# Kernel tuning notes

Measured on AMD Instinct MI355X. Metric: run time of the kernel, lower is better.

## Reference

```python
import jax, jax.numpy as jnp
import numpy as np

B, H, W, C = 8, 64, 64, 256
C8 = C // 8  # query/key channels


def setup_inputs() -> dict:
    key = jax.random.key(0)
    ks = jax.random.split(key, 8)
    s = 0.02  # init scale for weights
    return {
        "x": jax.random.normal(ks[0], (B, H, W, C), dtype=jnp.float32),
        "Wq": jax.random.normal(ks[1], (C, C8), dtype=jnp.float32) * s,
        "bq": jnp.zeros((C8,), dtype=jnp.float32),
        "Wk": jax.random.normal(ks[2], (C, C8), dtype=jnp.float32) * s,
        "bk": jnp.zeros((C8,), dtype=jnp.float32),
        "Wv": jax.random.normal(ks[3], (C, C), dtype=jnp.float32) * s,
        "bv": jnp.zeros((C,), dtype=jnp.float32),
        "gamma": jnp.full((1,), 0.5, dtype=jnp.float32),
    }


def reference(x, Wq, bq, Wk, bk, Wv, bv, gamma):
    Bn, Hn, Wn, Cn = x.shape
    N = Hn * Wn
    xf = x.reshape(Bn, N, Cn)            # flatten spatial dims: [B, N, C]
    # 1x1 convs == per-pixel dense projections over channels
    q = xf @ Wq + bq                     # [B, N, C//8]
    k = xf @ Wk + bk                     # [B, N, C//8]
    v = xf @ Wv + bv                     # [B, N, C]
    # energy[b,i,j] = k_i . q_j  (matches tf.matmul(key, query, transpose_b=True))
    energy = jnp.einsum('bic,bjc->bij', k, q)   # [B, N, N]
    attn = jax.nn.softmax(energy, axis=-1)      # softmax over last axis
    # out_i = sum_j attn[i,j] * v_j  (intended SAGAN aggregation in NHWC layout)
    out = jnp.einsum('bij,bjc->bic', attn, v)   # [B, N, C]
    out = out.reshape(Bn, Hn, Wn, Cn)
    return gamma * out + x
```

## Files before the change

kernel.cpp:

```cpp
#include <hip/hip_runtime.h>

typedef __attribute__((ext_vector_type(8))) short short8;
typedef __attribute__((ext_vector_type(4))) float f32x4;
typedef __attribute__((ext_vector_type(16))) float f32x16;
typedef __attribute__((ext_vector_type(2))) unsigned int u32x2;
typedef __attribute__((ext_vector_type(4))) unsigned int u32x4;
typedef unsigned short u16;
typedef unsigned int u32;

#define MFMA16(a, b, c) __builtin_amdgcn_mfma_f32_16x16x32_bf16((a), (b), (c), 0, 0, 0)
#define MFMA32(a, b, c) __builtin_amdgcn_mfma_f32_32x32x16_bf16((a), (b), (c), 0, 0, 0)

#define BAR_VMEM() asm volatile("s_waitcnt vmcnt(0) lgkmcnt(0)\ns_barrier" ::: "memory")
#define BAR_LDS()  asm volatile("s_waitcnt lgkmcnt(0)\ns_barrier" ::: "memory")

#define BATCH 8
#define NTOK 4096
#define CDIM 256
#define CQK 32
#define LOG2E 1.4426950408889634f

__device__ __forceinline__ u16 f2bf(float f) {
  u32 u = __float_as_uint(f);
  return (u16)((u + 0x7FFFu + ((u >> 16) & 1u)) >> 16);
}
__device__ __forceinline__ u32 pack2(float a, float b) {
  const u32 ua = __float_as_uint(a) + 0x8000u;
  const u32 ub = __float_as_uint(b) + 0x8000u;
#if __has_builtin(__builtin_amdgcn_perm)
  return __builtin_amdgcn_perm(ub, ua, 0x07060302u);
#else
  return (ua >> 16) | (ub & 0xFFFF0000u);
#endif
}
__device__ __forceinline__ float fexp2(float x) {
#if __has_builtin(__builtin_amdgcn_exp2f)
  return __builtin_amdgcn_exp2f(x);
#else
  return exp2f(x);
#endif
}
__device__ __forceinline__ void gl_lds16(const u16* g, u16* l) {
  __builtin_amdgcn_global_load_lds(
      (const __attribute__((address_space(1))) unsigned int*)(g),
      (__attribute__((address_space(3))) unsigned int*)(l), 16, 0, 0);
}

__global__ void k_prep(const float* __restrict__ Wq, const float* __restrict__ bq,
                       const float* __restrict__ Wk, const float* __restrict__ bk,
                       const float* __restrict__ Wv, const float* __restrict__ bv,
                       u16* __restrict__ wtf, float* __restrict__ bias) {
  const int f = blockIdx.x;
  const int L = threadIdx.x;
  const int ct = f >> 3, ks = f & 7;
  const int o = ct * 16 + (L & 15);
  const int ch = ks * 32 + (L >> 4) * 8;
  short8 v8;
#pragma unroll
  for (int jj = 0; jj < 8; jj++) {
    const int c = ch + jj;
    float v;
    if (o < 32)       v = Wq[c * CQK + o];
    else if (o < 64)  v = Wk[c * CQK + (o - 32)];
    else              v = Wv[c * CDIM + (o - 64)];
    v8[jj] = (short)f2bf(v);
  }
  *(short8*)(wtf + (size_t)f * 512 + L * 8) = v8;
  if (f == 0) {
    for (int i = L; i < 320; i += 64) {
      if (i < 32)      bias[i] = bq[i];
      else if (i < 64) bias[i] = bk[i - 32];
      else             bias[i] = bv[i - 64];
    }
  }
}

__global__ __launch_bounds__(256, 2) void k_proj(
    const float* __restrict__ x, const u16* __restrict__ wtf,
    const float* __restrict__ bias,
    u16* __restrict__ q_ws, u16* __restrict__ k_ws, u16* __restrict__ vt_ws) {
  __shared__ u16 x_lds[64 * 264];
  __shared__ u16 vt_t[64 * 72];
  const int m0 = blockIdx.x * 64;
  const int tid = threadIdx.x;
  const int w = tid >> 6, L = tid & 63;
  const int lr = L & 15, q4 = L >> 4;

#pragma unroll
  for (int ii = 0; ii < 8; ii++) {
    const int e = (tid + 256 * ii) * 8;
    const int row = e >> 8, col = e & 255;
    const float* src = x + (size_t)(m0 + row) * CDIM + col;
    f32x4 a = *(const f32x4*)src;
    f32x4 b4 = *(const f32x4*)(src + 4);
    u32x4 pk;
    pk[0] = pack2(a[0], a[1]);
    pk[1] = pack2(a[2], a[3]);
    pk[2] = pack2(b4[0], b4[1]);
    pk[3] = pack2(b4[2], b4[3]);
    *(u32x4*)&x_lds[row * 264 + col] = pk;
  }
  __syncthreads();

  const int mrow = w * 16;
  f32x4 acc[20];
#pragma unroll
  for (int ct = 0; ct < 20; ct++) acc[ct] = (f32x4){0.f, 0.f, 0.f, 0.f};

#pragma unroll
  for (int ks = 0; ks < 8; ks++) {
    short8 a = *(const short8*)&x_lds[(mrow + lr) * 264 + ks * 32 + q4 * 8];
#pragma unroll
    for (int ct = 0; ct < 20; ct++) {
      short8 bf = *(const short8*)(wtf + ((size_t)(ct * 8 + ks)) * 512 + L * 8);
      acc[ct] = MFMA16(a, bf, acc[ct]);
    }
  }

#pragma unroll
  for (int ct = 0; ct < 4; ct++) {
    const float bb = bias[ct * 16 + lr];
    const int o = ct * 16 + lr;
#pragma unroll
    for (int r = 0; r < 4; r++) {
      const int row = m0 + mrow + q4 * 4 + r;
      float v = acc[ct][r] + bb;
      if (o < 32) q_ws[(size_t)row * CQK + o] = f2bf(v);
      else        k_ws[(size_t)row * CQK + (o - 32)] = f2bf(v * LOG2E);
    }
  }
  const int b = m0 >> 12, nloc = m0 & 4095;
  const int rb2 = ((lr >> 3) & 1) << 2;
#pragma unroll
  for (int cg = 0; cg < 4; cg++) {
    __syncthreads();
#pragma unroll
    for (int t4 = 0; t4 < 4; t4++) {
      const int ct = 4 + cg * 4 + t4;
      const float bb = bias[ct * 16 + lr];
      const int c_l = t4 * 16 + lr;
      const int n_base = (mrow + q4 * 4) ^ rb2;
      u32x2 pk;
      pk[0] = pack2(acc[ct][0] + bb, acc[ct][1] + bb);
      pk[1] = pack2(acc[ct][2] + bb, acc[ct][3] + bb);
      *(u32x2*)&vt_t[c_l * 72 + n_base] = pk;
    }
    __syncthreads();
#pragma unroll
    for (int i = 0; i < 2; i++) {
      const int gch = tid + 256 * i;
      const int c_l = gch >> 3, jc = gch & 7;
      short8 v = *(const short8*)&vt_t[c_l * 72 + jc * 8];
      *(short8*)(vt_ws + ((size_t)(b * CDIM + cg * 64 + c_l)) * NTOK + nloc + jc * 8) = v;
    }
  }
}

__global__ __launch_bounds__(256, 4) void k_attn(
    const float* __restrict__ x, const u16* __restrict__ q_ws,
    const u16* __restrict__ k_ws, const u16* __restrict__ vt_ws,
    const float* __restrict__ gamma, float* __restrict__ out) {
  __shared__ u16 vt_lds[2][128 * 64];
  __shared__ u16 p_lds[64 * 64];

  const int bid = blockIdx.x;
  const int b = bid & 7;
  const int chalf = (bid >> 3) & 1;
  const int it = bid >> 4;
  const int i0 = it * 64;
  const int c0 = chalf * 128;
  const int tid = threadIdx.x;
  const int w = tid >> 6, L = tid & 63;
  const int lr = L & 15, q4 = L >> 4;
  const int L31 = L & 31, Lhi = L >> 5, L7 = L & 7;
  const int ih = w & 1, cpair = w >> 1;

  const short8 a_k = *(const short8*)(k_ws +
      ((size_t)(b * NTOK + i0 + w * 16 + lr)) * CQK + q4 * 8);

  const int cl_base = tid >> 3;
  const int jc_sw = (tid & 7) ^ (cl_base & 7);
  const u16* vt_g = vt_ws + ((size_t)(b * CDIM + c0 + cl_base)) * NTOK + jc_sw * 8;
  const u16* q_base = q_ws + (size_t)b * NTOK * CQK;

  f32x16 o_acc[2];
#pragma unroll
  for (int t = 0; t < 2; t++)
#pragma unroll
    for (int e = 0; e < 16; e++) o_acc[t][e] = 0.f;
  float lsum = 0.f;

  u16* pw0 = p_lds + (w * 16 + lr) * 64 + (((q4 & 1) ^ ((lr >> 3) & 1)) << 2);
  const int q4h = q4 >> 1;

  short8 bqA[4], bqB[4];
#pragma unroll
  for (int t = 0; t < 4; t++)
    bqA[t] = *(const short8*)(q_base + (size_t)(t * 16 + lr) * CQK + q4 * 8);
#pragma unroll
  for (int ii = 0; ii < 4; ii++)
    gl_lds16(vt_g + (size_t)(ii * 32) * NTOK, &vt_lds[0][ii * 2048 + w * 512]);

#define ATTN_ITER(JT, VB_CUR, VB_NXT, BQ, BQN)                                   \
  do {                                                                           \
    const int j0 = (JT) * 64;                                                    \
    BAR_LDS();                         \
       \
    _Pragma("unroll")                                                            \
    for (int t = 0; t < 4; t++)                                                  \
      BQN[t] = *(const short8*)(q_base +                                         \
               (size_t)(j0 + 64 + t * 16 + lr) * CQK + q4 * 8);                  \
                  \
    f32x4 s[4];                                                                  \
    _Pragma("unroll")                                                            \
    for (int t = 0; t < 4; t++)                                                  \
      s[t] = MFMA16(BQ[t], a_k, ((f32x4){0.f, 0.f, 0.f, 0.f}));                  \
                   \
    _Pragma("unroll")                                                            \
    for (int t = 0; t < 4; t++) {                                                \
      const float p0 = fexp2(s[t][0]);                                           \
      const float p1 = fexp2(s[t][1]);                                           \
      const float p2 = fexp2(s[t][2]);                                           \
      const float p3 = fexp2(s[t][3]);                                           \
      lsum += (p0 + p1) + (p2 + p3);                                             \
      u32x2 pk;                                                                  \
      pk[0] = pack2(p0, p1);                                                     \
      pk[1] = pack2(p2, p3);                                                     \
      *(u32x2*)(pw0 + (((2 * t + q4h) ^ (lr & 7)) * 8)) = pk;                    \
    }                                                                            \
    BAR_VMEM();          \
              \
    if ((JT) < 63) {                                                             \
      _Pragma("unroll")                                                          \
      for (int ii = 0; ii < 4; ii++)                                             \
        gl_lds16(vt_g + (size_t)(ii * 32) * NTOK + (j0 + 64),                    \
                 &VB_NXT[ii * 2048 + w * 512]);                                  \
    }                                                                            \
            \
    _Pragma("unroll")                                                            \
    for (int ks = 0; ks < 4; ks++) {                                             \
      const int slot = (((ks * 2 + Lhi) ^ L7)) * 8;                              \
      short8 a_p = *(const short8*)(p_lds + (ih * 32 + L31) * 64 + slot);        \
      _Pragma("unroll")                                                          \
      for (int ct2 = 0; ct2 < 2; ct2++) {                                        \
        const int cl = (cpair * 2 + ct2) * 32 + L31;                             \
        short8 b_v = *(const short8*)(&VB_CUR[0] + cl * 64 + slot);              \
        o_acc[ct2] = MFMA32(a_p, b_v, o_acc[ct2]);                               \
      }                                                                          \
    }                                                                            \
  } while (0)

  for (int jt2 = 0; jt2 < 64; jt2 += 2) {
    ATTN_ITER(jt2,     vt_lds[0], vt_lds[1], bqA, bqB);
    ATTN_ITER(jt2 + 1, vt_lds[1], vt_lds[0], bqB, bqA);
  }
#undef ATTN_ITER

  float s2 = lsum;
  s2 += __shfl_xor(s2, 16);
  s2 += __shfl_xor(s2, 32);
  const float rl = 1.0f / s2;
  BAR_LDS();
  float* lp = (float*)p_lds;
  if (q4 == 0) lp[w * 16 + lr] = rl;
  BAR_LDS();

  float linv[16];
#pragma unroll
  for (int rg = 0; rg < 16; rg++)
    linv[rg] = lp[ih * 32 + (rg & 3) + 8 * (rg >> 2) + 4 * Lhi];

  const float g = gamma[0];
#pragma unroll
  for (int ct2 = 0; ct2 < 2; ct2++) {
    const int c = c0 + (cpair * 2 + ct2) * 32 + L31;
#pragma unroll
    for (int rg = 0; rg < 16; rg++) {
      const int i = i0 + ih * 32 + (rg & 3) + 8 * (rg >> 2) + 4 * Lhi;
      const size_t idx = ((size_t)(b * NTOK + i)) * CDIM + c;
      out[idx] = g * (o_acc[ct2][rg] * linv[rg]) + x[idx];
    }
  }
}

extern "C" void kernel_launch(void* const* d_in, const int* in_sizes, int n_in,
                              void* d_out, int out_size, void* d_ws, size_t ws_size,
                              hipStream_t stream) {
  const float* x  = (const float*)d_in[0];
  const float* Wq = (const float*)d_in[1];
  const float* bq = (const float*)d_in[2];
  const float* Wk = (const float*)d_in[3];
  const float* bk = (const float*)d_in[4];
  const float* Wv = (const float*)d_in[5];
  const float* bv = (const float*)d_in[6];
  const float* gamma = (const float*)d_in[7];
  float* out = (float*)d_out;

  char* ws = (char*)d_ws;
  u16* q_ws  = (u16*)(ws);
  u16* k_ws  = (u16*)(ws + (2u << 20));
  u16* vt_ws = (u16*)(ws + (4u << 20));
  u16* wtf   = (u16*)(ws + (20u << 20));
  float* bias = (float*)(ws + (20u << 20) + (256u << 10));

  k_prep<<<160, 64, 0, stream>>>(Wq, bq, Wk, bk, Wv, bv, wtf, bias);
  k_proj<<<512, 256, 0, stream>>>(x, wtf, bias, q_ws, k_ws, vt_ws);
  k_attn<<<1024, 256, 0, stream>>>(x, q_ws, k_ws, vt_ws, gamma, out);
}
```

Baseline: 221.3 us.

## Repartition projection GEMM so each wave owns output columns and prefetches weights

The projection kernel now gives each wave a slice of output channels across all 64 rows, instead of 16 rows across all 320 output channels. Each wave therefore loads only its 5 weight fragments per k-step rather than 20, cutting redundant global weight traffic by 4x. Weight fragments are double-buffered in registers, with the first step loaded before the x staging so global latency overlaps. The cost is more LDS reads of the x tile (4 per k-step instead of 1) and a different register-pressure profile.

```diff
diff --git a/kernel.cpp b/kernel.cpp
--- a/kernel.cpp
+++ b/kernel.cpp
@@ -85,6 +85,11 @@
   const int tid = threadIdx.x;
   const int w = tid >> 6, L = tid & 63;
   const int lr = L & 15, q4 = L >> 4;
+
+  short8 wfA[5], wfB[5];
+#pragma unroll
+  for (int j = 0; j < 5; j++)
+    wfA[j] = *(const short8*)(wtf + ((size_t)((j * 4 + w) * 8 + 0)) * 512 + L * 8);
 
 #pragma unroll
   for (int ii = 0; ii < 8; ii++) {
@@ -102,56 +107,66 @@
   }
   __syncthreads();
 
-  const int mrow = w * 16;
-  f32x4 acc[20];
-#pragma unroll
-  for (int ct = 0; ct < 20; ct++) acc[ct] = (f32x4){0.f, 0.f, 0.f, 0.f};
+  f32x4 acc[4][5];
+#pragma unroll
+  for (int rg = 0; rg < 4; rg++)
+#pragma unroll
+    for (int j = 0; j < 5; j++) acc[rg][j] = (f32x4){0.f, 0.f, 0.f, 0.f};
 
 #pragma unroll
   for (int ks = 0; ks < 8; ks++) {
-    short8 a = *(const short8*)&x_lds[(mrow + lr) * 264 + ks * 32 + q4 * 8];
-#pragma unroll
-    for (int ct = 0; ct < 20; ct++) {
-      short8 bf = *(const short8*)(wtf + ((size_t)(ct * 8 + ks)) * 512 + L * 8);
-      acc[ct] = MFMA16(a, bf, acc[ct]);
-    }
-  }
-
-#pragma unroll
-  for (int ct = 0; ct < 4; ct++) {
-    const float bb = bias[ct * 16 + lr];
-    const int o = ct * 16 + lr;
-#pragma unroll
-    for (int r = 0; r < 4; r++) {
-      const int row = m0 + mrow + q4 * 4 + r;
-      float v = acc[ct][r] + bb;
-      if (o < 32) q_ws[(size_t)row * CQK + o] = f2bf(v);
-      else        k_ws[(size_t)row * CQK + (o - 32)] = f2bf(v * LOG2E);
-    }
+    if (ks < 7) {
+#pragma unroll
+      for (int j = 0; j < 5; j++) {
+        short8 v = *(const short8*)(wtf +
+            ((size_t)((j * 4 + w) * 8 + ks + 1)) * 512 + L * 8);
+        if (ks & 1) wfA[j] = v; else wfB[j] = v;
+      }
+    }
+#pragma unroll
+    for (int rg = 0; rg < 4; rg++) {
+      short8 a = *(const short8*)&x_lds[(rg * 16 + lr) * 264 + ks * 32 + q4 * 8];
+#pragma unroll
+      for (int j = 0; j < 5; j++)
+        acc[rg][j] = MFMA16(a, (ks & 1) ? wfB[j] : wfA[j], acc[rg][j]);
+    }
+  }
+
+  {
+    const float bb = bias[w * 16 + lr];
+#pragma unroll
+    for (int rg = 0; rg < 4; rg++)
+#pragma unroll
+      for (int r = 0; r < 4; r++) {
+        const int row = m0 + rg * 16 + q4 * 4 + r;
+        float v = acc[rg][0][r] + bb;
+        if (w < 2) q_ws[(size_t)row * CQK + w * 16 + lr] = f2bf(v);
+        else       k_ws[(size_t)row * CQK + (w - 2) * 16 + lr] = f2bf(v * LOG2E);
+      }
   }
   const int b = m0 >> 12, nloc = m0 & 4095;
   const int rb2 = ((lr >> 3) & 1) << 2;
+  const int c_l = w * 16 + lr;
 #pragma unroll
   for (int cg = 0; cg < 4; cg++) {
     __syncthreads();
-#pragma unroll
-    for (int t4 = 0; t4 < 4; t4++) {
-      const int ct = 4 + cg * 4 + t4;
-      const float bb = bias[ct * 16 + lr];
-      const int c_l = t4 * 16 + lr;
-      const int n_base = (mrow + q4 * 4) ^ rb2;
+    const int j = cg + 1;
+    const float bb = bias[(4 + cg * 4 + w) * 16 + lr];
+#pragma unroll
+    for (int rg = 0; rg < 4; rg++) {
+      const int n_base = (rg * 16 + q4 * 4) ^ rb2;
       u32x2 pk;
-      pk[0] = pack2(acc[ct][0] + bb, acc[ct][1] + bb);
-      pk[1] = pack2(acc[ct][2] + bb, acc[ct][3] + bb);
+      pk[0] = pack2(acc[rg][j][0] + bb, acc[rg][j][1] + bb);
+      pk[1] = pack2(acc[rg][j][2] + bb, acc[rg][j][3] + bb);
       *(u32x2*)&vt_t[c_l * 72 + n_base] = pk;
     }
     __syncthreads();
 #pragma unroll
     for (int i = 0; i < 2; i++) {
       const int gch = tid + 256 * i;
-      const int c_l = gch >> 3, jc = gch & 7;
-      short8 v = *(const short8*)&vt_t[c_l * 72 + jc * 8];
-      *(short8*)(vt_ws + ((size_t)(b * CDIM + cg * 64 + c_l)) * NTOK + nloc + jc * 8) = v;
+      const int cl2 = gch >> 3, jc = gch & 7;
+      short8 v = *(const short8*)&vt_t[cl2 * 72 + jc * 8];
+      *(short8*)(vt_ws + ((size_t)(b * CDIM + cg * 64 + cl2)) * NTOK + nloc + jc * 8) = v;
     }
   }
 }
```

After: 214.1 us. -3.3%, faster.
